# Kernel tuning notes

Hardware: AMD Instinct MI355X
Metric: run time of the kernel (lower is better)

Reference implementation:

```python
import jax, jax.numpy as jnp
import numpy as np

N = 100000      # nodes
E = 1600000     # edges (before self-loops)
IN = 256        # in_channels
HID = 16        # num_hid (per-head channels, layer 1)
HEADS = 4
OUT = 16        # out_channels (per-head channels, layer 2)
NEG_SLOPE = 0.2 # PyG GATConv default


def setup_inputs() -> dict:
    key = jax.random.key(0)
    ks = jax.random.split(key, 12)
    def glorot(k, shape, fan):
        return jax.random.normal(k, shape, jnp.float32) * (1.0 / np.sqrt(fan))
    x = jax.random.normal(ks[0], (N, IN), jnp.float32)
    edge_index = jax.random.randint(ks[1], (2, E), 0, N, dtype=jnp.int32)
    W1 = glorot(ks[2], (IN, HEADS * HID), IN)
    att_src1 = glorot(ks[3], (HEADS, HID), HID)
    att_dst1 = glorot(ks[4], (HEADS, HID), HID)
    b1 = jnp.zeros((HEADS * HID,), jnp.float32)
    W2 = glorot(ks[5], (HEADS * HID, HEADS * OUT), HEADS * HID)
    att_src2 = glorot(ks[6], (HEADS, OUT), OUT)
    att_dst2 = glorot(ks[7], (HEADS, OUT), OUT)
    b2 = jnp.zeros((HEADS * OUT,), jnp.float32)
    return {"x": x, "edge_index": edge_index, "W1": W1, "att_src1": att_src1,
            "att_dst1": att_dst1, "b1": b1, "W2": W2, "att_src2": att_src2,
            "att_dst2": att_dst2, "b2": b2}


def gat_conv(x, W, att_src, att_dst, bias, src, dst):
    # PyG GATConv (concat=True): h = xW per head; alpha via segment-softmax over dst.
    H, C = att_src.shape
    n = x.shape[0]
    h = (x @ W).reshape(n, H, C)                    # [N,H,C]
    a_s = jnp.sum(h * att_src, axis=-1)             # [N,H]
    a_d = jnp.sum(h * att_dst, axis=-1)             # [N,H]
    e = jax.nn.leaky_relu(a_s[src] + a_d[dst], NEG_SLOPE)  # [E',H]
    m = jax.lax.stop_gradient(jax.ops.segment_max(e, dst, num_segments=n))
    p = jnp.exp(e - m[dst])
    s = jax.ops.segment_sum(p, dst, num_segments=n)
    alpha = p / (s[dst] + 1e-16)                    # [E',H]
    msg = h[src] * alpha[:, :, None]                # [E',H,C] gathered messages
    out = jax.ops.segment_sum(msg, dst, num_segments=n)
    return out.reshape(n, H * C) + bias


def reference(x, edge_index, W1, att_src1, att_dst1, b1, W2, att_src2, att_dst2, b2):
    # add self loops (PyG GATConv default add_self_loops=True)
    loops = jnp.arange(N, dtype=edge_index.dtype)
    src = jnp.concatenate([edge_index[0], loops])
    dst = jnp.concatenate([edge_index[1], loops])
    h = jax.nn.relu(gat_conv(x, W1, att_src1, att_dst1, b1, src, dst))
    # dropout is identity in eval mode
    return gat_conv(h, W2, att_src2, att_dst2, b2, src, dst)
```

## Files before the change

kernel.cpp:

```cpp
#include <hip/hip_runtime.h>
#include <hip/hip_fp16.h>
#include <cstdint>


#define CH 4096
#define MAXB 512
#define SCAP 6144

using f16x8 = __attribute__((ext_vector_type(8))) _Float16;
using f32x4 = __attribute__((ext_vector_type(4))) float;

__device__ __forceinline__ float lrelu(float v) { return fmaxf(v, 0.2f * v); }

__global__ void ifill_kernel(int* __restrict__ p, int v, int n) {
  int i = blockIdx.x * blockDim.x + threadIdx.x;
  if (i < n) p[i] = v;
}

__global__ void wprep2_kernel(const float* __restrict__ W,
                              const float* __restrict__ as,
                              const float* __restrict__ ad,
                              ushort* __restrict__ WT, int K) {
  int i = blockIdx.x * 256 + threadIdx.x;
  if (i >= 80 * K) return;
  int c = i / K, k = i % K;
  float v = 0.f;
  if (c < 64) {
    v = W[k * 64 + c];
  } else if (c < 68) {
    int hd = c - 64;
    for (int j = 0; j < 16; ++j) v += W[k * 64 + hd * 16 + j] * as[hd * 16 + j];
  } else if (c < 72) {
    int hd = c - 68;
    for (int j = 0; j < 16; ++j) v += W[k * 64 + hd * 16 + j] * ad[hd * 16 + j];
  }
  WT[c * K + k] = __half_as_ushort(__float2half_rn(v));
}

__global__ __launch_bounds__(256) void bucket_hist(const int* __restrict__ edst,
                                                   int E, int nbuck,
                                                   int* __restrict__ bucket_cnt) {
  __shared__ int hist[MAXB];
  const int t = threadIdx.x;
  for (int j = t; j < MAXB; j += 256) hist[j] = 0;
  __syncthreads();
  const int base = blockIdx.x * CH;
#pragma unroll
  for (int k = 0; k < CH / 256; ++k) {
    int e = base + k * 256 + t;
    if (e < E) atomicAdd(&hist[edst[e] >> 8], 1);
  }
  __syncthreads();
  for (int j = t; j < nbuck; j += 256) {
    int c = hist[j];
    if (c) atomicAdd(&bucket_cnt[j], c);
  }
}

__global__ __launch_bounds__(512) void bucket_scan(const int* __restrict__ bucket_cnt,
                                                   int* __restrict__ bucket_base,
                                                   int* __restrict__ bucket_cursor,
                                                   int nbuck) {
  __shared__ int part[512];
  const int t = threadIdx.x;
  int v = (t < nbuck) ? bucket_cnt[t] : 0;
  part[t] = v;
  __syncthreads();
  for (int off = 1; off < 512; off <<= 1) {
    int u = (t >= off) ? part[t - off] : 0;
    __syncthreads();
    part[t] += u;
    __syncthreads();
  }
  int ex = part[t] - v;
  if (t <= nbuck) {
    int w = (t < nbuck) ? ex : part[nbuck - 1];
    bucket_base[t] = w;
    if (t < nbuck) bucket_cursor[t] = w;
  }
}

__global__ __launch_bounds__(256) void place_kernel(const int* __restrict__ esrc,
                                                    const int* __restrict__ edst,
                                                    int E, int nbuck,
                                                    int* __restrict__ bucket_cursor,
                                                    unsigned int* __restrict__ pairs) {
  __shared__ int hist[MAXB];
  __shared__ int gbase[MAXB];
  __shared__ int rcnt[MAXB];
  const int t = threadIdx.x;
  for (int j = t; j < MAXB; j += 256) { hist[j] = 0; rcnt[j] = 0; }
  __syncthreads();
  const int base = blockIdx.x * CH;
  int b_[CH / 256];
  unsigned int p_[CH / 256];
#pragma unroll
  for (int k = 0; k < CH / 256; ++k) {
    int e = base + k * 256 + t;
    if (e < E) {
      int d = edst[e];
      int s = esrc[e];
      b_[k] = d >> 8;
      p_[k] = ((unsigned int)s << 8) | (unsigned int)(d & 255);
      atomicAdd(&hist[b_[k]], 1);
    } else {
      b_[k] = -1;
    }
  }
  __syncthreads();
  for (int j = t; j < nbuck; j += 256) {
    int c = hist[j];
    gbase[j] = c ? atomicAdd(&bucket_cursor[j], c) : 0;
  }
  __syncthreads();
#pragma unroll
  for (int k = 0; k < CH / 256; ++k) {
    if (b_[k] >= 0) {
      int r = atomicAdd(&rcnt[b_[k]], 1);
      pairs[gbase[b_[k]] + r] = p_[k];
    }
  }
}

__global__ __launch_bounds__(256) void bucket_build(
    const unsigned int* __restrict__ pairs, const int* __restrict__ bucket_base,
    int* __restrict__ ccol, int* __restrict__ start, int* __restrict__ endp,
    int n) {
  __shared__ int cnt[256];
  __shared__ int ls[256];
  __shared__ int csave[256];
  __shared__ int part[256];
  __shared__ int sorted[SCAP];
  const int t = threadIdx.x;
  const int b = blockIdx.x;
  const int d0 = b << 8;
  const int DR = min(256, n - d0);
  const int in_base = bucket_base[b];
  const int nloc = bucket_base[b + 1] - in_base;
  const int out_base = in_base + d0;

  cnt[t] = (t < DR) ? 1 : 0;
  __syncthreads();
  for (int i = t; i < nloc; i += 256)
    atomicAdd(&cnt[pairs[in_base + i] & 255u], 1);
  __syncthreads();
  int c = cnt[t];
  csave[t] = c;
  part[t] = c;
  __syncthreads();
#pragma unroll
  for (int off = 1; off < 256; off <<= 1) {
    int u = (t >= off) ? part[t - off] : 0;
    __syncthreads();
    part[t] += u;
    __syncthreads();
  }
  ls[t] = part[t] - c;
  __syncthreads();
  if (t < DR) {
    int s = out_base + ls[t];
    start[d0 + t] = s;
    endp[d0 + t] = s + csave[t];
    sorted[ls[t]] = d0 + t;
    cnt[t] = 1;
  }
  __syncthreads();
  for (int i = t; i < nloc; i += 256) {
    unsigned int p = pairs[in_base + i];
    int j = (int)(p & 255u);
    int r = atomicAdd(&cnt[j], 1);
    int pos = ls[j] + r;
    if (pos < SCAP) sorted[pos] = (int)(p >> 8);
  }
  __syncthreads();
  int tot = nloc + DR;
  if (tot > SCAP) tot = SCAP;
  for (int i = t; i < tot; i += 256) ccol[out_base + i] = sorted[i];
}

__global__ __launch_bounds__(256) void gemm1_mfma(
    const float* __restrict__ x, const ushort* __restrict__ wt,
    __half* __restrict__ h, float* __restrict__ as_, float* __restrict__ ad_,
    int n) {
  constexpr int K = 256, NS = K / 32;
  __shared__ _Float16 hs[64 * 88];
  __shared__ float att[64 * 12];
  const int tid = threadIdx.x;
  const int w = tid >> 6;
  const int lane = tid & 63;
  const int lr = lane & 15;
  const int kg = lane >> 4;
  const int row0 = blockIdx.x * 64;

  int rr = row0 + w * 16 + lr;
  if (rr > n - 1) rr = n - 1;

  const ushort* wbase = wt + lr * K + kg * 8;

  f16x8 af[NS];
  {
    float4 av[NS][2];
    const float* xp = x + (long long)rr * K + kg * 8;
#pragma unroll
    for (int s = 0; s < NS; ++s) {
      av[s][0] = *(const float4*)(xp + s * 32);
      av[s][1] = *(const float4*)(xp + s * 32 + 4);
    }
#pragma unroll
    for (int s = 0; s < NS; ++s) {
      af[s][0] = (_Float16)av[s][0].x; af[s][1] = (_Float16)av[s][0].y;
      af[s][2] = (_Float16)av[s][0].z; af[s][3] = (_Float16)av[s][0].w;
      af[s][4] = (_Float16)av[s][1].x; af[s][5] = (_Float16)av[s][1].y;
      af[s][6] = (_Float16)av[s][1].z; af[s][7] = (_Float16)av[s][1].w;
    }
  }

  f32x4 acc[5] = {};
#pragma unroll
  for (int s = 0; s < NS; ++s)
#pragma unroll
    for (int ct = 0; ct < 5; ++ct) {
      f16x8 b = *(const f16x8*)(wbase + ct * 16 * K + s * 32);
      acc[ct] = __builtin_amdgcn_mfma_f32_16x16x32_f16(af[s], b, acc[ct], 0, 0, 0);
    }

  const int orow = w * 16 + kg * 4;
#pragma unroll
  for (int ct = 0; ct < 4; ++ct)
#pragma unroll
    for (int r = 0; r < 4; ++r)
      hs[(orow + r) * 88 + ct * 16 + lr] = (_Float16)acc[ct][r];
  if (lr < 8) {
#pragma unroll
    for (int r = 0; r < 4; ++r)
      att[(orow + r) * 12 + lr] = acc[4][r];
  }
  __syncthreads();
#pragma unroll
  for (int j = 0; j < 2; ++j) {
    int s = tid + j * 256;
    int row = s >> 3, seg = s & 7;
    if (row0 + row < n)
      *(uint4*)(h + (long long)(row0 + row) * 64 + seg * 8) =
          *(const uint4*)&hs[row * 88 + seg * 8];
  }
  if (tid < 64) {
    if (row0 + tid < n)
      *(float4*)(as_ + (long long)(row0 + tid) * 4) = *(const float4*)&att[tid * 12];
  } else if (tid < 128) {
    int t2 = tid - 64;
    if (row0 + t2 < n)
      *(float4*)(ad_ + (long long)(row0 + t2) * 4) = *(const float4*)&att[t2 * 12 + 4];
  }
}

__global__ __launch_bounds__(320) void agg1_kernel(
    const int* __restrict__ ccol, const int* __restrict__ start,
    const int* __restrict__ endp,
    const float* __restrict__ as1, const float* __restrict__ ad1,
    const __half2* __restrict__ h2in, const float* __restrict__ bias,
    const ushort* __restrict__ wt2,
    __half* __restrict__ h2out, float* __restrict__ as2,
    float* __restrict__ ad2, int n) {
  __shared__ _Float16 x2s[16 * 72];
  __shared__ _Float16 hs2[16 * 72];
  __shared__ float att2[16 * 12];
  const int t = threadIdx.x;

  for (int i = t; i < 6 * 72; i += 320) x2s[10 * 72 + i] = (_Float16)0.f;
  if (t < 80) x2s[(t >> 3) * 72 + 64 + (t & 7)] = (_Float16)0.f;

  const int lw = t >> 5;
  const int hl = t & 31;
  const int hh = hl >> 3;
  const int node = blockIdx.x * 10 + lw;
  const bool act = node < n;
  const int nodec = act ? node : 0;

  const float adv = ad1[nodec * 4 + hh];
  const int s0i = start[nodec];
  const int d = act ? (endp[nodec] - s0i) : 0;
  const int* cp = ccol + s0i;
  float ax = 0.f, ay = 0.f, den = 0.f;
  int i = 0;
  for (; i + 4 <= d; i += 4) {
    int s0 = cp[i], s1 = cp[i + 1], s2 = cp[i + 2], s3 = cp[i + 3];
    float p0 = __expf(lrelu(as1[s0 * 4 + hh] + adv));
    float p1 = __expf(lrelu(as1[s1 * 4 + hh] + adv));
    float p2 = __expf(lrelu(as1[s2 * 4 + hh] + adv));
    float p3 = __expf(lrelu(as1[s3 * 4 + hh] + adv));
    float2 h0 = __half22float2(h2in[s0 * 32 + hl]);
    float2 h1 = __half22float2(h2in[s1 * 32 + hl]);
    float2 h2v = __half22float2(h2in[s2 * 32 + hl]);
    float2 h3 = __half22float2(h2in[s3 * 32 + hl]);
    den += (p0 + p1) + (p2 + p3);
    ax = fmaf(p0, h0.x, ax); ay = fmaf(p0, h0.y, ay);
    ax = fmaf(p1, h1.x, ax); ay = fmaf(p1, h1.y, ay);
    ax = fmaf(p2, h2v.x, ax); ay = fmaf(p2, h2v.y, ay);
    ax = fmaf(p3, h3.x, ax); ay = fmaf(p3, h3.y, ay);
  }
  for (; i < d; ++i) {
    int s0 = cp[i];
    float p0 = __expf(lrelu(as1[s0 * 4 + hh] + adv));
    float2 h0 = __half22float2(h2in[s0 * 32 + hl]);
    den += p0;
    ax = fmaf(p0, h0.x, ax); ay = fmaf(p0, h0.y, ay);
  }
  const float inv = 1.0f / (den + 1e-16f);
  float vx = act ? fmaxf(ax * inv + bias[hl * 2], 0.f) : 0.f;
  float vy = act ? fmaxf(ay * inv + bias[hl * 2 + 1], 0.f) : 0.f;
  x2s[lw * 72 + hl * 2] = (_Float16)vx;
  x2s[lw * 72 + hl * 2 + 1] = (_Float16)vy;
  __syncthreads();

  {
    const int w = t >> 6;
    const int lane = t & 63;
    const int lr = lane & 15;
    const int kg = lane >> 4;
    const ushort* wb = wt2 + (w * 16 + lr) * 64 + kg * 8;
    f32x4 acc = {};
#pragma unroll
    for (int s = 0; s < 2; ++s) {
      f16x8 a = *(const f16x8*)&x2s[lr * 72 + s * 32 + kg * 8];
      f16x8 b = *(const f16x8*)(wb + s * 32);
      acc = __builtin_amdgcn_mfma_f32_16x16x32_f16(a, b, acc, 0, 0, 0);
    }
    if (w < 4) {
#pragma unroll
      for (int r = 0; r < 4; ++r)
        hs2[(kg * 4 + r) * 72 + w * 16 + lr] = (_Float16)acc[r];
    } else if (lr < 8) {
#pragma unroll
      for (int r = 0; r < 4; ++r)
        att2[(kg * 4 + r) * 12 + lr] = acc[r];
    }
  }
  __syncthreads();

  if (t < 80) {
    int row = t >> 3, seg = t & 7;
    int gn = blockIdx.x * 10 + row;
    if (gn < n)
      *(uint4*)(h2out + (long long)gn * 64 + seg * 8) =
          *(const uint4*)&hs2[row * 72 + seg * 8];
  } else if (t < 90) {
    int row = t - 80;
    int gn = blockIdx.x * 10 + row;
    if (gn < n) *(float4*)(as2 + (long long)gn * 4) = *(const float4*)&att2[row * 12];
  } else if (t < 100) {
    int row = t - 90;
    int gn = blockIdx.x * 10 + row;
    if (gn < n) *(float4*)(ad2 + (long long)gn * 4) = *(const float4*)&att2[row * 12 + 4];
  }
}

__global__ __launch_bounds__(256) void agg2_kernel(
    const int* __restrict__ ccol, const int* __restrict__ start,
    const int* __restrict__ endp,
    const float* __restrict__ as2, const float* __restrict__ ad2,
    const __half2* __restrict__ h2, const float* __restrict__ bias,
    float* __restrict__ out, int n) {
  const int node = blockIdx.x * 8 + (threadIdx.x >> 5);
  if (node >= n) return;
  const int hl = threadIdx.x & 31;
  const int hh = hl >> 3;
  const float adv = ad2[node * 4 + hh];
  const int s0i = start[node];
  const int d = endp[node] - s0i;
  const int* cp = ccol + s0i;
  float ax = 0.f, ay = 0.f, den = 0.f;
  int i = 0;
  for (; i + 4 <= d; i += 4) {
    int s0 = cp[i], s1 = cp[i + 1], s2 = cp[i + 2], s3 = cp[i + 3];
    float p0 = __expf(lrelu(as2[s0 * 4 + hh] + adv));
    float p1 = __expf(lrelu(as2[s1 * 4 + hh] + adv));
    float p2 = __expf(lrelu(as2[s2 * 4 + hh] + adv));
    float p3 = __expf(lrelu(as2[s3 * 4 + hh] + adv));
    float2 h0 = __half22float2(h2[s0 * 32 + hl]);
    float2 h1 = __half22float2(h2[s1 * 32 + hl]);
    float2 h2v = __half22float2(h2[s2 * 32 + hl]);
    float2 h3 = __half22float2(h2[s3 * 32 + hl]);
    den += (p0 + p1) + (p2 + p3);
    ax = fmaf(p0, h0.x, ax); ay = fmaf(p0, h0.y, ay);
    ax = fmaf(p1, h1.x, ax); ay = fmaf(p1, h1.y, ay);
    ax = fmaf(p2, h2v.x, ax); ay = fmaf(p2, h2v.y, ay);
    ax = fmaf(p3, h3.x, ax); ay = fmaf(p3, h3.y, ay);
  }
  for (; i < d; ++i) {
    int s0 = cp[i];
    float p0 = __expf(lrelu(as2[s0 * 4 + hh] + adv));
    float2 h0 = __half22float2(h2[s0 * 32 + hl]);
    den += p0;
    ax = fmaf(p0, h0.x, ax); ay = fmaf(p0, h0.y, ay);
  }
  const float inv = 1.0f / (den + 1e-16f);
  float vx = ax * inv + bias[hl * 2];
  float vy = ay * inv + bias[hl * 2 + 1];
  *(float2*)(out + (long long)node * 64 + hl * 2) = make_float2(vx, vy);
}

extern "C" void kernel_launch(void* const* d_in, const int* in_sizes, int n_in,
                              void* d_out, int out_size, void* d_ws, size_t ws_size,
                              hipStream_t stream) {
  const float* x = (const float*)d_in[0];
  const int* ei = (const int*)d_in[1];
  const float* W1 = (const float*)d_in[2];
  const float* att_s1 = (const float*)d_in[3];
  const float* att_d1 = (const float*)d_in[4];
  const float* b1 = (const float*)d_in[5];
  const float* W2 = (const float*)d_in[6];
  const float* att_s2 = (const float*)d_in[7];
  const float* att_d2 = (const float*)d_in[8];
  const float* b2 = (const float*)d_in[9];

  const int n = in_sizes[0] / 256;
  const int E = in_sizes[1] / 2;
  const int* esrc = ei;
  const int* edst = ei + E;
  const int nbuck = (n + 255) >> 8;

  float* wsf = (float*)d_ws;
  __half* hbuf = (__half*)wsf;
  __half* h2buf = (__half*)(wsf + (long long)n * 32);
  float* as1 = wsf + (long long)n * 64;
  float* ad1 = as1 + (long long)n * 4;
  float* as2 = ad1 + (long long)n * 4;
  float* ad2 = as2 + (long long)n * 4;
  int* bucket_cnt = (int*)(ad2 + (long long)n * 4);
  int* bucket_base = bucket_cnt + MAXB;
  int* bucket_cursor = bucket_base + MAXB + 1;
  int* start = bucket_cursor + MAXB;
  int* endp = start + n;
  unsigned int* pairs = (unsigned int*)(endp + n);
  int* ccol = (int*)(pairs + E);
  ushort* wt1 = (ushort*)(((uintptr_t)(ccol + E + n) + 15) & ~(uintptr_t)15);
  ushort* wt2 = wt1 + 80 * 256;
  float* out = (float*)d_out;

  const int ebk = (E + CH - 1) / CH;
  const int gb = (n + 63) / 64;
  const int nb1 = (n + 9) / 10;
  const int nb2 = (n + 7) / 8;

  wprep2_kernel<<<(80 * 256 + 255) / 256, 256, 0, stream>>>(W1, att_s1, att_d1, wt1, 256);
  wprep2_kernel<<<(80 * 64 + 255) / 256, 256, 0, stream>>>(W2, att_s2, att_d2, wt2, 64);

  ifill_kernel<<<(MAXB + 255) / 256, 256, 0, stream>>>(bucket_cnt, 0, MAXB);
  bucket_hist<<<ebk, 256, 0, stream>>>(edst, E, nbuck, bucket_cnt);
  bucket_scan<<<1, 512, 0, stream>>>(bucket_cnt, bucket_base, bucket_cursor, nbuck);
  place_kernel<<<ebk, 256, 0, stream>>>(esrc, edst, E, nbuck, bucket_cursor, pairs);
  bucket_build<<<nbuck, 256, 0, stream>>>(pairs, bucket_base, ccol, start, endp, n);

  gemm1_mfma<<<gb, 256, 0, stream>>>(x, wt1, hbuf, as1, ad1, n);
  agg1_kernel<<<nb1, 320, 0, stream>>>(ccol, start, endp, as1, ad1,
                                       (const __half2*)hbuf, b1, wt2,
                                       h2buf, as2, ad2, n);

  agg2_kernel<<<nb2, 256, 0, stream>>>(ccol, start, endp, as2, ad2,
                                       (const __half2*)h2buf, b2, out, n);
}
```

Before: 234.3 us.

## Sort nodes by descending degree before aggregation kernels for load balance

Adds a counting sort of nodes by in-degree (histogram, scan, place) and builds a permutation. Both aggregation kernels then process nodes in permuted order, so each block handles nodes of similar degree and warps within a block spend less time idle waiting on a high-degree neighbour. The cost is four extra small launches, an indirection through perm, and scattered writes of outputs by node id that lose locality.

```diff
diff --git a/kernel.cpp b/kernel.cpp
--- a/kernel.cpp
+++ b/kernel.cpp
@@ -178,6 +178,51 @@
   for (int i = t; i < tot; i += 256) ccol[out_base + i] = sorted[i];
 }
 
+__global__ __launch_bounds__(256) void deg_hist_kernel(
+    const int* __restrict__ start, const int* __restrict__ endp, int n,
+    int* __restrict__ dcnt) {
+  __shared__ int h[128];
+  if (threadIdx.x < 128) h[threadIdx.x] = 0;
+  __syncthreads();
+  int v = blockIdx.x * 256 + threadIdx.x;
+  if (v < n) {
+    int dg = endp[v] - start[v];
+    if (dg > 127) dg = 127;
+    atomicAdd(&h[127 - dg], 1);
+  }
+  __syncthreads();
+  if (threadIdx.x < 128 && h[threadIdx.x])
+    atomicAdd(&dcnt[threadIdx.x], h[threadIdx.x]);
+}
+
+__global__ __launch_bounds__(128) void deg_scan_kernel(const int* __restrict__ dcnt,
+                                                       int* __restrict__ dcur) {
+  __shared__ int part[128];
+  const int t = threadIdx.x;
+  int v = dcnt[t];
+  part[t] = v;
+  __syncthreads();
+  for (int off = 1; off < 128; off <<= 1) {
+    int u = (t >= off) ? part[t - off] : 0;
+    __syncthreads();
+    part[t] += u;
+    __syncthreads();
+  }
+  dcur[t] = part[t] - v;
+}
+
+__global__ __launch_bounds__(256) void deg_place_kernel(
+    const int* __restrict__ start, const int* __restrict__ endp, int n,
+    int* __restrict__ dcur, int* __restrict__ perm) {
+  int v = blockIdx.x * 256 + threadIdx.x;
+  if (v < n) {
+    int dg = endp[v] - start[v];
+    if (dg > 127) dg = 127;
+    int pos = atomicAdd(&dcur[127 - dg], 1);
+    perm[pos] = v;
+  }
+}
+
 __global__ __launch_bounds__(256) void gemm1_mfma(
     const float* __restrict__ x, const ushort* __restrict__ wt,
     __half* __restrict__ h, float* __restrict__ as_, float* __restrict__ ad_,
@@ -256,7 +301,7 @@
 
 __global__ __launch_bounds__(320) void agg1_kernel(
     const int* __restrict__ ccol, const int* __restrict__ start,
-    const int* __restrict__ endp,
+    const int* __restrict__ endp, const int* __restrict__ perm,
     const float* __restrict__ as1, const float* __restrict__ ad1,
     const __half2* __restrict__ h2in, const float* __restrict__ bias,
     const ushort* __restrict__ wt2,
@@ -273,13 +318,13 @@
   const int lw = t >> 5;
   const int hl = t & 31;
   const int hh = hl >> 3;
-  const int node = blockIdx.x * 10 + lw;
-  const bool act = node < n;
-  const int nodec = act ? node : 0;
-
-  const float adv = ad1[nodec * 4 + hh];
-  const int s0i = start[nodec];
-  const int d = act ? (endp[nodec] - s0i) : 0;
+  const int slot = blockIdx.x * 10 + lw;
+  const bool act = slot < n;
+  const int node = act ? perm[slot] : 0;
+
+  const float adv = ad1[node * 4 + hh];
+  const int s0i = start[node];
+  const int d = act ? (endp[node] - s0i) : 0;
   const int* cp = ccol + s0i;
   float ax = 0.f, ay = 0.f, den = 0.f;
   int i = 0;
@@ -340,29 +385,38 @@
 
   if (t < 80) {
     int row = t >> 3, seg = t & 7;
-    int gn = blockIdx.x * 10 + row;
-    if (gn < n)
+    int s2_ = blockIdx.x * 10 + row;
+    if (s2_ < n) {
+      int gn = perm[s2_];
       *(uint4*)(h2out + (long long)gn * 64 + seg * 8) =
           *(const uint4*)&hs2[row * 72 + seg * 8];
+    }
   } else if (t < 90) {
     int row = t - 80;
-    int gn = blockIdx.x * 10 + row;
-    if (gn < n) *(float4*)(as2 + (long long)gn * 4) = *(const float4*)&att2[row * 12];
+    int s2_ = blockIdx.x * 10 + row;
+    if (s2_ < n) {
+      int gn = perm[s2_];
+      *(float4*)(as2 + (long long)gn * 4) = *(const float4*)&att2[row * 12];
+    }
   } else if (t < 100) {
     int row = t - 90;
-    int gn = blockIdx.x * 10 + row;
-    if (gn < n) *(float4*)(ad2 + (long long)gn * 4) = *(const float4*)&att2[row * 12 + 4];
+    int s2_ = blockIdx.x * 10 + row;
+    if (s2_ < n) {
+      int gn = perm[s2_];
+      *(float4*)(ad2 + (long long)gn * 4) = *(const float4*)&att2[row * 12 + 4];
+    }
   }
 }
 
 __global__ __launch_bounds__(256) void agg2_kernel(
     const int* __restrict__ ccol, const int* __restrict__ start,
-    const int* __restrict__ endp,
+    const int* __restrict__ endp, const int* __restrict__ perm,
     const float* __restrict__ as2, const float* __restrict__ ad2,
     const __half2* __restrict__ h2, const float* __restrict__ bias,
     float* __restrict__ out, int n) {
-  const int node = blockIdx.x * 8 + (threadIdx.x >> 5);
-  if (node >= n) return;
+  const int slot = blockIdx.x * 8 + (threadIdx.x >> 5);
+  if (slot >= n) return;
+  const int node = perm[slot];
   const int hl = threadIdx.x & 31;
   const int hh = hl >> 3;
   const float adv = ad2[node * 4 + hh];
@@ -436,12 +490,16 @@
   int* ccol = (int*)(pairs + E);
   ushort* wt1 = (ushort*)(((uintptr_t)(ccol + E + n) + 15) & ~(uintptr_t)15);
   ushort* wt2 = wt1 + 80 * 256;
+  int* dcnt = (int*)(wt2 + 80 * 64);
+  int* dcur = dcnt + 128;
+  int* perm = dcur + 128;
   float* out = (float*)d_out;
 
   const int ebk = (E + CH - 1) / CH;
   const int gb = (n + 63) / 64;
   const int nb1 = (n + 9) / 10;
   const int nb2 = (n + 7) / 8;
+  const int vb = (n + 255) / 256;
 
   wprep2_kernel<<<(80 * 256 + 255) / 256, 256, 0, stream>>>(W1, att_s1, att_d1, wt1, 256);
   wprep2_kernel<<<(80 * 64 + 255) / 256, 256, 0, stream>>>(W2, att_s2, att_d2, wt2, 64);
@@ -452,11 +510,16 @@
   place_kernel<<<ebk, 256, 0, stream>>>(esrc, edst, E, nbuck, bucket_cursor, pairs);
   bucket_build<<<nbuck, 256, 0, stream>>>(pairs, bucket_base, ccol, start, endp, n);
 
+  ifill_kernel<<<1, 128, 0, stream>>>(dcnt, 0, 128);
+  deg_hist_kernel<<<vb, 256, 0, stream>>>(start, endp, n, dcnt);
+  deg_scan_kernel<<<1, 128, 0, stream>>>(dcnt, dcur);
+  deg_place_kernel<<<vb, 256, 0, stream>>>(start, endp, n, dcur, perm);
+
   gemm1_mfma<<<gb, 256, 0, stream>>>(x, wt1, hbuf, as1, ad1, n);
-  agg1_kernel<<<nb1, 320, 0, stream>>>(ccol, start, endp, as1, ad1,
+  agg1_kernel<<<nb1, 320, 0, stream>>>(ccol, start, endp, perm, as1, ad1,
                                        (const __half2*)hbuf, b1, wt2,
                                        h2buf, as2, ad2, n);
 
-  agg2_kernel<<<nb2, 256, 0, stream>>>(ccol, start, endp, as2, ad2,
+  agg2_kernel<<<nb2, 256, 0, stream>>>(ccol, start, endp, perm, as2, ad2,
                                        (const __half2*)h2buf, b2, out, n);
 }
```

Measured after the change: 523.9 us. +123.6%, slower.
